# Kernel optimization log

Measured on AMD Instinct MI355X. Metric: run time of the kernel, lower is better.

## Reference

```python
import jax, jax.numpy as jnp
import numpy as np

N, IN, H, OUT, C = 1024, 64, 64, 64, 32
EPS = 1e-5   # SAKELayer.epsilon
INF = 1e5    # SAKELayer.inf


def _w(key, i, o, scale=1.0):
    return jax.random.normal(key, (i, o), jnp.float32) * (scale / np.sqrt(i))


def setup_inputs() -> dict:
    key = jax.random.key(0)
    ks = jax.random.split(key, 16)
    return dict(
        h=jax.random.normal(ks[0], (N, IN), jnp.float32),
        x=jax.random.normal(ks[1], (N, 3), jnp.float32),
        # edge model (ConcatenationFilter): Linear(2*IN+1,H), SiLU, Linear(H,H)
        ew1=_w(ks[2], 2 * IN + 1, H), eb1=jnp.zeros((H,), jnp.float32),
        ew2=_w(ks[3], H, H), eb2=jnp.zeros((H,), jnp.float32),
        # node_mlp: Linear(2H+IN,H), SiLU, Linear(H,OUT)
        nw1=_w(ks[4], 2 * H + IN, H), nb1=jnp.zeros((H,), jnp.float32),
        nw2=_w(ks[5], H, OUT), nb2=jnp.zeros((OUT,), jnp.float32),
        # coordinate_mlp: Linear(H,H), SiLU, Linear(H,1,bias=False) xavier gain 1e-3
        cw1=_w(ks[6], H, H), cb1=jnp.zeros((H,), jnp.float32),
        cw2=_w(ks[7], H, 1, scale=1e-3),
        # semantic_attention_mlp: Linear(H,1), LeakyReLU
        aw=_w(ks[8], H, 1), ab=jnp.zeros((1,), jnp.float32),
        # coefficients_mlp: Linear(H,H), SiLU, Linear(H,C)
        fw1=_w(ks[9], H, H), fb1=jnp.zeros((H,), jnp.float32),
        fw2=_w(ks[10], H, C), fb2=jnp.zeros((C,), jnp.float32),
        # post_norm_mlp: Linear(C,H), SiLU, Linear(H,H)
        pw1=_w(ks[11], C, H), pb1=jnp.zeros((H,), jnp.float32),
        pw2=_w(ks[12], H, H), pb2=jnp.zeros((H,), jnp.float32),
        log_gamma=jnp.array(0.0, jnp.float32),
    )


def reference(h, x, ew1, eb1, ew2, eb2, nw1, nb1, nw2, nb2, cw1, cb1, cw2,
              aw, ab, fw1, fb1, fw2, fb2, pw1, pb1, pw2, pb2, log_gamma):
    n, d_in = h.shape
    silu = jax.nn.silu
    eye = jnp.eye(n, dtype=h.dtype)[:, :, None]                    # [n,n,1]

    x_minus_xt = x[:, None, :] - x[None, :, :]                     # [n,n,3]
    norm = jnp.sqrt(jnp.sum(x_minus_xt ** 2, -1, keepdims=True) + EPS)  # [n,n,1]

    h_cat_ht = jnp.concatenate(
        [jnp.broadcast_to(h[:, None, :], (n, n, d_in)),
         jnp.broadcast_to(h[None, :, :], (n, n, d_in))], -1)       # [n,n,2*IN]

    # edge model: MLP over concat(features, distance)
    e_in = jnp.concatenate([h_cat_ht, norm], -1)                   # [n,n,2*IN+1]
    h_e = silu(e_in @ ew1 + eb1) @ ew2 + eb2                       # [n,n,H]

    # euclidean attention over neighbors j (diag masked by +INF distance)
    att_e = jax.nn.softmax(-(norm + INF * eye) * jnp.exp(log_gamma), axis=1)
    # semantic attention
    att_s = jax.nn.softmax(jax.nn.leaky_relu(h_e @ aw + ab) - INF * eye, axis=1)
    comb = att_e * att_s
    comb = comb / (jnp.sum(comb, axis=1, keepdims=True) + EPS)     # [n,n,1]
    h_e_att = h_e * comb                                           # [n,n,H]

    # spatial attention: equivariant coefficient combinations
    coeff = silu(h_e_att @ fw1 + fb1) @ fw2 + fb2                  # [n,n,C]
    dirs = x_minus_xt / (norm + 1.0)                               # [n,n,3]
    combos = jnp.einsum('ijc,ijd->icd', coeff, dirs) / n           # mean over j -> [n,C,3]
    h_comb = silu(jnp.sum(combos ** 2, -1) @ pw1 + pb1) @ pw2 + pb2  # [n,H]

    # node update
    h_agg = jnp.sum(h_e_att, axis=1)                               # [n,H]
    node_in = jnp.concatenate([h, h_agg, h_comb], -1)              # [n,2H+IN]
    h_out = h + (silu(node_in @ nw1 + nb1) @ nw2 + nb2)            # residual

    # equivariant coordinate update
    phi = silu(h_e @ cw1 + cb1) @ cw2                              # [n,n,1]
    x_out = x + jnp.mean(x_minus_xt * phi, axis=1)                 # [n,3]
    return h_out, x_out
```

## Files before the change

### kernel.cpp

```cpp
#include <hip/hip_runtime.h>
#include <hip/hip_bf16.h>

#define NN 1024
#define LSTR 72
#define EPSV 1e-5f
#define BIGINF 1e5f

typedef __attribute__((ext_vector_type(8))) short short8;
typedef __attribute__((ext_vector_type(4))) short short4v;
typedef __attribute__((ext_vector_type(4))) float f32x4;

__device__ __forceinline__ float siluf(float v) {
    return v * __builtin_amdgcn_rcpf(1.0f + __expf(-v));
}
__device__ __forceinline__ float pnorm(float dx, float dy, float dz) {
    return sqrtf(dx * dx + dy * dy + dz * dz + EPSV);
}
__device__ __forceinline__ float wsum(float v) {
#pragma unroll
    for (int off = 32; off > 0; off >>= 1) v += __shfl_xor(v, off, 64);
    return v;
}
__device__ __forceinline__ float red16(float v) {
    v += __shfl_xor(v, 1, 64); v += __shfl_xor(v, 2, 64);
    v += __shfl_xor(v, 4, 64); v += __shfl_xor(v, 8, 64);
    return v;
}
__device__ __forceinline__ float redquad(float v) {
    v += __shfl_xor(v, 16, 64); v += __shfl_xor(v, 32, 64);
    return v;
}
__device__ __forceinline__ short f2bs(float v) {
    __hip_bfloat16 b = __float2bfloat16(v);
    return *reinterpret_cast<short*>(&b);
}
__device__ __forceinline__ short f2bt(float v) {
    return (short)(__float_as_uint(v) >> 16);
}

__global__ void kA(const float* __restrict__ h, const float* __restrict__ ew1,
                   const float* __restrict__ eb1, const float* __restrict__ ew2,
                   const float* __restrict__ cw1, const float* __restrict__ fw1,
                   const float* __restrict__ fw2, const float* __restrict__ aw,
                   const float* __restrict__ ab, const float* __restrict__ eb2,
                   float* __restrict__ HA, float* __restrict__ HB,
                   float* __restrict__ HBT, short* __restrict__ ew2T,
                   short* __restrict__ cw1T, short* __restrict__ fw1T,
                   short* __restrict__ fw2T, float* __restrict__ wsv,
                   float* __restrict__ svb) {
    const int b = blockIdx.x;
    const int o = threadIdx.x;
    if (b < NN) {
        const int i = b;
        float hv = h[i * 64 + o];
        float a = 0.f, bb = eb1[o];
#pragma unroll
        for (int k = 0; k < 64; k++) {
            float hk = __shfl(hv, k, 64);
            a += hk * ew1[k * 64 + o];
            bb += hk * ew1[(64 + k) * 64 + o];
        }
        HA[i * 64 + o] = a;
        HB[i * 64 + o] = bb;
        HBT[o * NN + i] = bb;
    } else if (b < NN + 64) {
        const int r = b - NN;
        ew2T[r * 64 + o] = f2bs(ew2[o * 64 + r]);
        cw1T[r * 64 + o] = f2bs(cw1[o * 64 + r]);
        fw1T[r * 64 + o] = f2bs(fw1[o * 64 + r]);
        if (r < 32) fw2T[r * 64 + o] = f2bs(fw2[o * 32 + r]);
    } else {
        float s = 0.f;
#pragma unroll
        for (int q = 0; q < 64; q++) s += ew2[o * 64 + q] * aw[q];
        wsv[o] = s;
        float e = wsum(eb2[o] * aw[o]);
        if (o == 0) svb[0] = e + ab[0];
    }
}

__global__ __launch_bounds__(256) void kBn(
    const float* __restrict__ x, const float* __restrict__ ew1,
    const float* __restrict__ HA, const float* __restrict__ HBT,
    const float* __restrict__ wsv, const float* __restrict__ svb,
    const float* __restrict__ lg, float* __restrict__ ls,
    float* __restrict__ rowm, float* __restrict__ rowd) {
    const int i = blockIdx.x;
    const int t = threadIdx.x;
    const float* HAi = HA + i * 64;
    const float* w1 = ew1 + 128 * 64;
    const float gamma = __expf(lg[0]);
    const float svb0 = svb[0];
    const float xi0 = x[i * 3 + 0], xi1 = x[i * 3 + 1], xi2 = x[i * 3 + 2];

    float4 xa = ((const float4*)x)[3 * t + 0];
    float4 xb = ((const float4*)x)[3 * t + 1];
    float4 xc = ((const float4*)x)[3 * t + 2];
    float nrm[4], le[4], lv[4];
    {
        float dx0 = xi0 - xa.x, dy0 = xi1 - xa.y, dz0 = xi2 - xa.z;
        float dx1 = xi0 - xa.w, dy1 = xi1 - xb.x, dz1 = xi2 - xb.y;
        float dx2 = xi0 - xb.z, dy2 = xi1 - xb.w, dz2 = xi2 - xc.x;
        float dx3 = xi0 - xc.y, dy3 = xi1 - xc.z, dz3 = xi2 - xc.w;
        nrm[0] = pnorm(dx0, dy0, dz0);
        nrm[1] = pnorm(dx1, dy1, dz1);
        nrm[2] = pnorm(dx2, dy2, dz2);
        nrm[3] = pnorm(dx3, dy3, dz3);
    }
    float d0 = 0.f, d1 = 0.f, d2 = 0.f, d3 = 0.f;
#pragma unroll 8
    for (int k = 0; k < 64; k++) {
        float4 hb = *(const float4*)&HBT[k * NN + 4 * t];
        float hk = HAi[k], w1k = w1[k], wv = wsv[k];
        d0 += siluf(hk + hb.x + nrm[0] * w1k) * wv;
        d1 += siluf(hk + hb.y + nrm[1] * w1k) * wv;
        d2 += siluf(hk + hb.z + nrm[2] * w1k) * wv;
        d3 += siluf(hk + hb.w + nrm[3] * w1k) * wv;
    }
    float me = -3.0e38f, ms = -3.0e38f;
    float4 svo;
    {
        float dd[4] = {d0, d1, d2, d3};
#pragma unroll
        for (int m = 0; m < 4; m++) {
            int j = 4 * t + m;
            float sv = dd[m] + svb0;
            sv = sv >= 0.f ? sv : 0.01f * sv;
            if (j == i) sv -= BIGINF;
            lv[m] = sv;
            le[m] = -(nrm[m] + (j == i ? BIGINF : 0.f)) * gamma;
            me = fmaxf(me, le[m]);
            ms = fmaxf(ms, lv[m]);
        }
        svo.x = lv[0]; svo.y = lv[1]; svo.z = lv[2]; svo.w = lv[3];
    }
    *(float4*)&ls[(size_t)i * NN + 4 * t] = svo;

    __shared__ float sm[4], ss[4], s1[4], s2[4], s3[4];
#pragma unroll
    for (int off = 32; off > 0; off >>= 1) {
        me = fmaxf(me, __shfl_xor(me, off, 64));
        ms = fmaxf(ms, __shfl_xor(ms, off, 64));
    }
    const int w = t >> 6;
    if ((t & 63) == 0) { sm[w] = me; ss[w] = ms; }
    __syncthreads();
    me = fmaxf(fmaxf(sm[0], sm[1]), fmaxf(sm[2], sm[3]));
    ms = fmaxf(fmaxf(ss[0], ss[1]), fmaxf(ss[2], ss[3]));
    float Se = 0.f, Ss = 0.f, Sq = 0.f;
#pragma unroll
    for (int m = 0; m < 4; m++) {
        float ee = __expf(le[m] - me);
        float es = __expf(lv[m] - ms);
        Se += ee; Ss += es; Sq += ee * es;
    }
    Se = wsum(Se); Ss = wsum(Ss); Sq = wsum(Sq);
    if ((t & 63) == 0) { s1[w] = Se; s2[w] = Ss; s3[w] = Sq; }
    __syncthreads();
    if (t == 0) {
        rowm[i] = me + ms;
        rowd[i] = (s3[0] + s3[1] + s3[2] + s3[3]) +
                  EPSV * (s1[0] + s1[1] + s1[2] + s1[3]) * (s2[0] + s2[1] + s2[2] + s2[3]);
    }
}

__device__ __forceinline__ void stageW(const short* __restrict__ g, short* s,
                                       int tid, int rows) {
    for (int c = tid; c < rows * 16; c += 512) {
        int r = c >> 4, q = c & 15;
        *(short4v*)&s[r * LSTR + q * 4] = *(const short4v*)&g[r * 64 + q * 4];
    }
}

__global__ __launch_bounds__(512) void kD(
    const float* __restrict__ x, const float* __restrict__ ew1,
    const float* __restrict__ eb2, const float* __restrict__ cb1,
    const float* __restrict__ cw2, const float* __restrict__ fb1,
    const float* __restrict__ fb2, const float* __restrict__ lg,
    const float* __restrict__ HA, const float* __restrict__ HB,
    const short* __restrict__ ew2T, const short* __restrict__ cw1T,
    const short* __restrict__ fw1T, const short* __restrict__ fw2T,
    const float* __restrict__ ls, const float* __restrict__ rowm,
    const float* __restrict__ rowd, float* __restrict__ hagg,
    float* __restrict__ combos, float* __restrict__ xupd) {
    __shared__ __align__(16) short sWe[64 * LSTR];
    __shared__ __align__(16) short sWf[64 * LSTR];
    __shared__ __align__(16) short sW2[32 * LSTR];
    __shared__ __align__(16) short sScr[16][16 * LSTR];
    __shared__ float sHag[64], sCombos[96], sXupd[3];

    const int tid = threadIdx.x;
    const int i = blockIdx.x;
    const int lane = tid & 63, w = tid >> 6;
    const int col = lane & 15, quad = lane >> 4;

    stageW(ew2T, sWe, tid, 64);
    stageW(fw1T, sWf, tid, 64);
    stageW(fw2T, sW2, tid, 32);
    if (tid < 64) sHag[tid] = 0.f;
    else if (tid < 160) sCombos[tid - 64] = 0.f;
    else if (tid < 163) sXupd[tid - 160] = 0.f;

    short* scr0 = sScr[2 * w];
    short* scr1 = sScr[2 * w + 1];
    const float gamma = __expf(lg[0]);

    float w1r[2][8], har[2][8];
#pragma unroll
    for (int kb = 0; kb < 2; kb++)
#pragma unroll
        for (int t = 0; t < 8; t++) {
            w1r[kb][t] = ew1[128 * 64 + kb * 32 + quad * 8 + t];
            har[kb][t] = HA[i * 64 + kb * 32 + quad * 8 + t];
        }
    float eb[4], cbv[4], cwv[4], fbv[4];
#pragma unroll
    for (int nb = 0; nb < 4; nb++) {
        eb[nb] = eb2[nb * 16 + col];
        cbv[nb] = cb1[nb * 16 + col];
        cwv[nb] = cw2[nb * 16 + col];
        fbv[nb] = fb1[nb * 16 + col];
    }
    float fb2v[2] = {fb2[col], fb2[16 + col]};
    const float rm = rowm[i];
    const float invd = 1.0f / rowd[i];
    const float xi0 = x[i * 3 + 0], xi1 = x[i * 3 + 1], xi2 = x[i * 3 + 2];
    const float* lsi = ls + (size_t)i * NN;
    __syncthreads();

#pragma unroll 1
    for (int jt = 0; jt < 4; jt++) {
        const int r0 = jt * 256 + w * 16 + col;
        const int r1 = r0 + 128;
        float dx0 = xi0 - x[r0 * 3 + 0], dy0 = xi1 - x[r0 * 3 + 1], dz0 = xi2 - x[r0 * 3 + 2];
        float dx1 = xi0 - x[r1 * 3 + 0], dy1 = xi1 - x[r1 * 3 + 1], dz1 = xi2 - x[r1 * 3 + 2];
        float nr0 = pnorm(dx0, dy0, dz0), nr1 = pnorm(dx1, dy1, dz1);
        float iv0 = __builtin_amdgcn_rcpf(nr0 + 1.0f), iv1 = __builtin_amdgcn_rcpf(nr1 + 1.0f);
        float fx0 = dx0 * iv0, fy0 = dy0 * iv0, fz0 = dz0 * iv0;
        float fx1 = dx1 * iv1, fy1 = dy1 * iv1, fz1 = dz1 * iv1;
        float le0 = -(nr0 + (r0 == i ? BIGINF : 0.f)) * gamma;
        float le1 = -(nr1 + (r1 == i ? BIGINF : 0.f)) * gamma;
        float cb0 = __expf(le0 + lsi[r0] - rm) * invd;
        float cb1f = __expf(le1 + lsi[r1] - rm) * invd;

        short8 af0[2], af1[2];
#pragma unroll
        for (int kb = 0; kb < 2; kb++) {
            const float* hb0 = &HB[r0 * 64 + kb * 32 + quad * 8];
            const float* hb1 = &HB[r1 * 64 + kb * 32 + quad * 8];
#pragma unroll
            for (int t = 0; t < 8; t++) {
                af0[kb][t] = f2bt(siluf(har[kb][t] + hb0[t] + nr0 * w1r[kb][t]));
                af1[kb][t] = f2bt(siluf(har[kb][t] + hb1[t] + nr1 * w1r[kb][t]));
            }
        }
        f32x4 ac0[4] = {{0.f,0.f,0.f,0.f},{0.f,0.f,0.f,0.f},{0.f,0.f,0.f,0.f},{0.f,0.f,0.f,0.f}};
        f32x4 ac1[4] = {{0.f,0.f,0.f,0.f},{0.f,0.f,0.f,0.f},{0.f,0.f,0.f,0.f},{0.f,0.f,0.f,0.f}};
#pragma unroll
        for (int kb = 0; kb < 2; kb++) {
#pragma unroll
            for (int nb = 0; nb < 4; nb++) {
                short8 b = *(const short8*)&sWe[(nb * 16 + col) * LSTR + kb * 32 + quad * 8];
                ac0[nb] = __builtin_amdgcn_mfma_f32_16x16x32_bf16(af0[kb], b, ac0[nb], 0, 0, 0);
                ac1[nb] = __builtin_amdgcn_mfma_f32_16x16x32_bf16(af1[kb], b, ac1[nb], 0, 0, 0);
            }
        }
        {
            float cm0[4], cm1[4];
#pragma unroll
            for (int reg = 0; reg < 4; reg++) {
                cm0[reg] = __shfl(cb0, quad * 4 + reg, 64);
                cm1[reg] = __shfl(cb1f, quad * 4 + reg, 64);
            }
#pragma unroll
            for (int nb = 0; nb < 4; nb++) {
                float v = 0.f;
#pragma unroll
                for (int reg = 0; reg < 4; reg++) {
                    float h0 = ac0[nb][reg] + eb[nb];
                    float h1 = ac1[nb][reg] + eb[nb];
                    scr0[(quad * 4 + reg) * LSTR + nb * 16 + col] = f2bt(h0);
                    scr1[(quad * 4 + reg) * LSTR + nb * 16 + col] = f2bt(h1);
                    v += h0 * cm0[reg] + h1 * cm1[reg];
                }
                v = redquad(v);
                if (quad == 0) atomicAdd(&sHag[nb * 16 + col], v);
            }
        }
        short8 a00 = *(const short8*)&scr0[col * LSTR + quad * 8];
        short8 a01 = *(const short8*)&scr0[col * LSTR + 32 + quad * 8];
        short8 a10 = *(const short8*)&scr1[col * LSTR + quad * 8];
        short8 a11 = *(const short8*)&scr1[col * LSTR + 32 + quad * 8];

        {
            f32x4 p0[4] = {{0.f,0.f,0.f,0.f},{0.f,0.f,0.f,0.f},{0.f,0.f,0.f,0.f},{0.f,0.f,0.f,0.f}};
            f32x4 p1[4] = {{0.f,0.f,0.f,0.f},{0.f,0.f,0.f,0.f},{0.f,0.f,0.f,0.f},{0.f,0.f,0.f,0.f}};
#pragma unroll
            for (int nb = 0; nb < 4; nb++) {
                short8 b0 = *(const short8*)&cw1T[(nb * 16 + col) * 64 + quad * 8];
                short8 b1 = *(const short8*)&cw1T[(nb * 16 + col) * 64 + 32 + quad * 8];
                p0[nb] = __builtin_amdgcn_mfma_f32_16x16x32_bf16(a00, b0, p0[nb], 0, 0, 0);
                p0[nb] = __builtin_amdgcn_mfma_f32_16x16x32_bf16(a01, b1, p0[nb], 0, 0, 0);
                p1[nb] = __builtin_amdgcn_mfma_f32_16x16x32_bf16(a10, b0, p1[nb], 0, 0, 0);
                p1[nb] = __builtin_amdgcn_mfma_f32_16x16x32_bf16(a11, b1, p1[nb], 0, 0, 0);
            }
            float xa0 = 0.f, xa1 = 0.f, xa2 = 0.f;
#pragma unroll
            for (int reg = 0; reg < 4; reg++) {
                float ph0 = 0.f, ph1 = 0.f;
#pragma unroll
                for (int nb = 0; nb < 4; nb++) {
                    ph0 += siluf(p0[nb][reg] + cbv[nb]) * cwv[nb];
                    ph1 += siluf(p1[nb][reg] + cbv[nb]) * cwv[nb];
                }
                ph0 = red16(ph0); ph1 = red16(ph1);
                float t0x = __shfl(dx0, quad * 4 + reg, 64);
                float t0y = __shfl(dy0, quad * 4 + reg, 64);
                float t0z = __shfl(dz0, quad * 4 + reg, 64);
                float t1x = __shfl(dx1, quad * 4 + reg, 64);
                float t1y = __shfl(dy1, quad * 4 + reg, 64);
                float t1z = __shfl(dz1, quad * 4 + reg, 64);
                if (col == 0) {
                    xa0 += ph0 * t0x + ph1 * t1x;
                    xa1 += ph0 * t0y + ph1 * t1y;
                    xa2 += ph0 * t0z + ph1 * t1z;
                }
            }
            xa0 = wsum(xa0); xa1 = wsum(xa1); xa2 = wsum(xa2);
            if (lane == 0) {
                atomicAdd(&sXupd[0], xa0);
                atomicAdd(&sXupd[1], xa1);
                atomicAdd(&sXupd[2], xa2);
            }
        }

        {
            f32x4 v0[4] = {{0.f,0.f,0.f,0.f},{0.f,0.f,0.f,0.f},{0.f,0.f,0.f,0.f},{0.f,0.f,0.f,0.f}};
            f32x4 v1[4] = {{0.f,0.f,0.f,0.f},{0.f,0.f,0.f,0.f},{0.f,0.f,0.f,0.f},{0.f,0.f,0.f,0.f}};
#pragma unroll
            for (int nb = 0; nb < 4; nb++) {
                short8 b0 = *(const short8*)&sWf[(nb * 16 + col) * LSTR + quad * 8];
                short8 b1 = *(const short8*)&sWf[(nb * 16 + col) * LSTR + 32 + quad * 8];
                v0[nb] = __builtin_amdgcn_mfma_f32_16x16x32_bf16(a00, b0, v0[nb], 0, 0, 0);
                v0[nb] = __builtin_amdgcn_mfma_f32_16x16x32_bf16(a01, b1, v0[nb], 0, 0, 0);
                v1[nb] = __builtin_amdgcn_mfma_f32_16x16x32_bf16(a10, b0, v1[nb], 0, 0, 0);
                v1[nb] = __builtin_amdgcn_mfma_f32_16x16x32_bf16(a11, b1, v1[nb], 0, 0, 0);
            }
            float cm0[4], cm1[4];
#pragma unroll
            for (int reg = 0; reg < 4; reg++) {
                cm0[reg] = __shfl(cb0, quad * 4 + reg, 64);
                cm1[reg] = __shfl(cb1f, quad * 4 + reg, 64);
            }
#pragma unroll
            for (int reg = 0; reg < 4; reg++) {
#pragma unroll
                for (int nb = 0; nb < 4; nb++) {
                    scr0[(quad * 4 + reg) * LSTR + nb * 16 + col] =
                        f2bt(siluf(cm0[reg] * v0[nb][reg] + fbv[nb]));
                    scr1[(quad * 4 + reg) * LSTR + nb * 16 + col] =
                        f2bt(siluf(cm1[reg] * v1[nb][reg] + fbv[nb]));
                }
            }
        }
        short8 wa00 = *(const short8*)&scr0[col * LSTR + quad * 8];
        short8 wa01 = *(const short8*)&scr0[col * LSTR + 32 + quad * 8];
        short8 wa10 = *(const short8*)&scr1[col * LSTR + quad * 8];
        short8 wa11 = *(const short8*)&scr1[col * LSTR + 32 + quad * 8];

        {
            f32x4 c0[2] = {{0.f,0.f,0.f,0.f},{0.f,0.f,0.f,0.f}};
            f32x4 c1[2] = {{0.f,0.f,0.f,0.f},{0.f,0.f,0.f,0.f}};
#pragma unroll
            for (int nb = 0; nb < 2; nb++) {
                short8 b0 = *(const short8*)&sW2[(nb * 16 + col) * LSTR + quad * 8];
                short8 b1 = *(const short8*)&sW2[(nb * 16 + col) * LSTR + 32 + quad * 8];
                c0[nb] = __builtin_amdgcn_mfma_f32_16x16x32_bf16(wa00, b0, c0[nb], 0, 0, 0);
                c0[nb] = __builtin_amdgcn_mfma_f32_16x16x32_bf16(wa01, b1, c0[nb], 0, 0, 0);
                c1[nb] = __builtin_amdgcn_mfma_f32_16x16x32_bf16(wa10, b0, c1[nb], 0, 0, 0);
                c1[nb] = __builtin_amdgcn_mfma_f32_16x16x32_bf16(wa11, b1, c1[nb], 0, 0, 0);
            }
#pragma unroll
            for (int nb = 0; nb < 2; nb++) {
                float px = 0.f, py = 0.f, pz = 0.f;
#pragma unroll
                for (int reg = 0; reg < 4; reg++) {
                    float cf0 = c0[nb][reg] + fb2v[nb];
                    float cf1 = c1[nb][reg] + fb2v[nb];
                    float t0x = __shfl(fx0, quad * 4 + reg, 64);
                    float t0y = __shfl(fy0, quad * 4 + reg, 64);
                    float t0z = __shfl(fz0, quad * 4 + reg, 64);
                    float t1x = __shfl(fx1, quad * 4 + reg, 64);
                    float t1y = __shfl(fy1, quad * 4 + reg, 64);
                    float t1z = __shfl(fz1, quad * 4 + reg, 64);
                    px += cf0 * t0x + cf1 * t1x;
                    py += cf0 * t0y + cf1 * t1y;
                    pz += cf0 * t0z + cf1 * t1z;
                }
                px = redquad(px); py = redquad(py); pz = redquad(pz);
                if (quad == 0) {
                    int c = nb * 16 + col;
                    atomicAdd(&sCombos[c * 3 + 0], px);
                    atomicAdd(&sCombos[c * 3 + 1], py);
                    atomicAdd(&sCombos[c * 3 + 2], pz);
                }
            }
        }
    }
    __syncthreads();
    if (tid < 64) hagg[i * 64 + tid] = sHag[tid];
    else if (tid < 160) combos[i * 96 + tid - 64] = sCombos[tid - 64];
    else if (tid < 163) xupd[i * 3 + tid - 160] = sXupd[tid - 160];
}

__global__ void kE(const float* __restrict__ h, const float* __restrict__ x,
                   const float* __restrict__ nw1, const float* __restrict__ nb1,
                   const float* __restrict__ nw2, const float* __restrict__ nb2,
                   const float* __restrict__ pw1, const float* __restrict__ pb1,
                   const float* __restrict__ pw2, const float* __restrict__ pb2,
                   const float* __restrict__ hagg, const float* __restrict__ combos,
                   const float* __restrict__ xupd, float* __restrict__ out) {
    const int i = blockIdx.x, o = threadIdx.x;
    const float invN = 1.0f / (float)NN;
    float r = 0.f;
    if (o < 32) {
        float v0 = combos[i * 96 + o * 3 + 0] * invN;
        float v1 = combos[i * 96 + o * 3 + 1] * invN;
        float v2 = combos[i * 96 + o * 3 + 2] * invN;
        r = v0 * v0 + v1 * v1 + v2 * v2;
    }
    float t1 = pb1[o];
#pragma unroll
    for (int k = 0; k < 32; k++) t1 += __shfl(r, k, 64) * pw1[k * 64 + o];
    t1 = siluf(t1);
    float hc = pb2[o];
#pragma unroll
    for (int k = 0; k < 64; k++) hc += __shfl(t1, k, 64) * pw2[k * 64 + o];
    float hi = h[i * 64 + o];
    float ha = hagg[i * 64 + o];
    float t2 = nb1[o];
#pragma unroll
    for (int k = 0; k < 64; k++) t2 += __shfl(hi, k, 64) * nw1[k * 64 + o];
#pragma unroll
    for (int k = 0; k < 64; k++) t2 += __shfl(ha, k, 64) * nw1[(64 + k) * 64 + o];
#pragma unroll
    for (int k = 0; k < 64; k++) t2 += __shfl(hc, k, 64) * nw1[(128 + k) * 64 + o];
    t2 = siluf(t2);
    float ho = hi + nb2[o];
#pragma unroll
    for (int k = 0; k < 64; k++) ho += __shfl(t2, k, 64) * nw2[k * 64 + o];
    out[i * 64 + o] = ho;
    if (o < 3)
        out[NN * 64 + i * 3 + o] = x[i * 3 + o] + xupd[i * 3 + o] * invN;
}

extern "C" void kernel_launch(void* const* d_in, const int* in_sizes, int n_in,
                              void* d_out, int out_size, void* d_ws, size_t ws_size,
                              hipStream_t stream) {
    (void)in_sizes; (void)n_in; (void)out_size; (void)ws_size;
    const float* h   = (const float*)d_in[0];
    const float* x   = (const float*)d_in[1];
    const float* ew1 = (const float*)d_in[2];
    const float* eb1 = (const float*)d_in[3];
    const float* ew2 = (const float*)d_in[4];
    const float* eb2 = (const float*)d_in[5];
    const float* nw1 = (const float*)d_in[6];
    const float* nb1 = (const float*)d_in[7];
    const float* nw2 = (const float*)d_in[8];
    const float* nb2 = (const float*)d_in[9];
    const float* cw1 = (const float*)d_in[10];
    const float* cb1 = (const float*)d_in[11];
    const float* cw2 = (const float*)d_in[12];
    const float* aw  = (const float*)d_in[13];
    const float* ab  = (const float*)d_in[14];
    const float* fw1 = (const float*)d_in[15];
    const float* fb1 = (const float*)d_in[16];
    const float* fw2 = (const float*)d_in[17];
    const float* fb2 = (const float*)d_in[18];
    const float* pw1 = (const float*)d_in[19];
    const float* pb1 = (const float*)d_in[20];
    const float* pw2 = (const float*)d_in[21];
    const float* pb2 = (const float*)d_in[22];
    const float* lg  = (const float*)d_in[23];
    float* out = (float*)d_out;

    float* W      = (float*)d_ws;
    float* ls     = W;
    float* HA     = ls + (size_t)NN * NN;
    float* HB     = HA + NN * 64;
    float* HBT    = HB + NN * 64;
    float* rowm   = HBT + NN * 64;
    float* rowd   = rowm + NN;
    float* hagg   = rowd + NN;
    float* combos = hagg + NN * 64;
    float* xupd   = combos + NN * 96;
    float* wsv    = xupd + NN * 3;
    float* svb    = wsv + 64;
    short* ew2T   = (short*)(svb + 4);
    short* cw1T   = ew2T + 64 * 64;
    short* fw1T   = cw1T + 64 * 64;
    short* fw2T   = fw1T + 64 * 64;

    kA<<<NN + 65, 64, 0, stream>>>(h, ew1, eb1, ew2, cw1, fw1, fw2, aw, ab, eb2,
                                   HA, HB, HBT, ew2T, cw1T, fw1T, fw2T, wsv, svb);
    kBn<<<NN, 256, 0, stream>>>(x, ew1, HA, HBT, wsv, svb, lg, ls, rowm, rowd);
    kD<<<NN, 512, 0, stream>>>(x, ew1, eb2, cb1, cw2, fb1, fb2, lg, HA, HB,
                               ew2T, cw1T, fw1T, fw2T, ls, rowm, rowd,
                               hagg, combos, xupd);
    kE<<<NN, 64, 0, stream>>>(h, x, nw1, nb1, nw2, nb2, pw1, pb1, pw2, pb2,
                              hagg, combos, xupd, out);
}
```

Before: 282.5 us.

## Factor final linear layers out of per-edge loop via linearity of sums

The last coefficient layer (fw2) and the coordinate output projection (cw2) are linear, so the change accumulates per-node sums of activations times direction vectors inside the edge loop. It then applies fw2/fb2 and cw2 once per node in the final kernel. This removes the per-edge fw2 MFMA pass, its scratch round-trip, and per-tile cross-lane reductions and shared atomics, which are now done once at loop end. In exchange it keeps more accumulator registers live (occupancy hinted via launch bounds), adds more shuffles per tile, and moves a small matvec into the last kernel.

```diff
diff --git a/kernel.cpp b/kernel.cpp
--- a/kernel.cpp
+++ b/kernel.cpp
@@ -19,11 +19,6 @@
 __device__ __forceinline__ float wsum(float v) {
 #pragma unroll
     for (int off = 32; off > 0; off >>= 1) v += __shfl_xor(v, off, 64);
-    return v;
-}
-__device__ __forceinline__ float red16(float v) {
-    v += __shfl_xor(v, 1, 64); v += __shfl_xor(v, 2, 64);
-    v += __shfl_xor(v, 4, 64); v += __shfl_xor(v, 8, 64);
     return v;
 }
 __device__ __forceinline__ float redquad(float v) {
@@ -172,22 +167,20 @@
     }
 }
 
-__global__ __launch_bounds__(512) void kD(
+__global__ __launch_bounds__(512, 4) void kD(
     const float* __restrict__ x, const float* __restrict__ ew1,
     const float* __restrict__ eb2, const float* __restrict__ cb1,
-    const float* __restrict__ cw2, const float* __restrict__ fb1,
-    const float* __restrict__ fb2, const float* __restrict__ lg,
+    const float* __restrict__ fb1, const float* __restrict__ lg,
     const float* __restrict__ HA, const float* __restrict__ HB,
     const short* __restrict__ ew2T, const short* __restrict__ cw1T,
-    const short* __restrict__ fw1T, const short* __restrict__ fw2T,
+    const short* __restrict__ fw1T,
     const float* __restrict__ ls, const float* __restrict__ rowm,
     const float* __restrict__ rowd, float* __restrict__ hagg,
-    float* __restrict__ combos, float* __restrict__ xupd) {
+    float* __restrict__ Gw, float* __restrict__ H2w, float* __restrict__ sdw) {
     __shared__ __align__(16) short sWe[64 * LSTR];
     __shared__ __align__(16) short sWf[64 * LSTR];
-    __shared__ __align__(16) short sW2[32 * LSTR];
     __shared__ __align__(16) short sScr[16][16 * LSTR];
-    __shared__ float sHag[64], sCombos[96], sXupd[3];
+    __shared__ float sHag[64], sG[192], sH2[192], sSd[3];
 
     const int tid = threadIdx.x;
     const int i = blockIdx.x;
@@ -196,36 +189,31 @@
 
     stageW(ew2T, sWe, tid, 64);
     stageW(fw1T, sWf, tid, 64);
-    stageW(fw2T, sW2, tid, 32);
     if (tid < 64) sHag[tid] = 0.f;
-    else if (tid < 160) sCombos[tid - 64] = 0.f;
-    else if (tid < 163) sXupd[tid - 160] = 0.f;
+    else if (tid < 256) sG[tid - 64] = 0.f;
+    else if (tid < 448) sH2[tid - 256] = 0.f;
+    else if (tid < 451) sSd[tid - 448] = 0.f;
 
     short* scr0 = sScr[2 * w];
     short* scr1 = sScr[2 * w + 1];
     const float gamma = __expf(lg[0]);
 
-    float w1r[2][8], har[2][8];
-#pragma unroll
-    for (int kb = 0; kb < 2; kb++)
-#pragma unroll
-        for (int t = 0; t < 8; t++) {
-            w1r[kb][t] = ew1[128 * 64 + kb * 32 + quad * 8 + t];
-            har[kb][t] = HA[i * 64 + kb * 32 + quad * 8 + t];
-        }
-    float eb[4], cbv[4], cwv[4], fbv[4];
+    float eb[4], cbv[4], fbv[4];
 #pragma unroll
     for (int nb = 0; nb < 4; nb++) {
         eb[nb] = eb2[nb * 16 + col];
         cbv[nb] = cb1[nb * 16 + col];
-        cwv[nb] = cw2[nb * 16 + col];
         fbv[nb] = fb1[nb * 16 + col];
     }
-    float fb2v[2] = {fb2[col], fb2[16 + col]};
     const float rm = rowm[i];
     const float invd = 1.0f / rowd[i];
     const float xi0 = x[i * 3 + 0], xi1 = x[i * 3 + 1], xi2 = x[i * 3 + 2];
     const float* lsi = ls + (size_t)i * NN;
+
+    float hagA[4] = {0.f, 0.f, 0.f, 0.f};
+    float Ga[12]  = {0.f, 0.f, 0.f, 0.f, 0.f, 0.f, 0.f, 0.f, 0.f, 0.f, 0.f, 0.f};
+    float H2a[12] = {0.f, 0.f, 0.f, 0.f, 0.f, 0.f, 0.f, 0.f, 0.f, 0.f, 0.f, 0.f};
+    float sdx = 0.f, sdy = 0.f, sdz = 0.f;
     __syncthreads();
 
 #pragma unroll 1
@@ -236,8 +224,9 @@
         float dx1 = xi0 - x[r1 * 3 + 0], dy1 = xi1 - x[r1 * 3 + 1], dz1 = xi2 - x[r1 * 3 + 2];
         float nr0 = pnorm(dx0, dy0, dz0), nr1 = pnorm(dx1, dy1, dz1);
         float iv0 = __builtin_amdgcn_rcpf(nr0 + 1.0f), iv1 = __builtin_amdgcn_rcpf(nr1 + 1.0f);
-        float fx0 = dx0 * iv0, fy0 = dy0 * iv0, fz0 = dz0 * iv0;
-        float fx1 = dx1 * iv1, fy1 = dy1 * iv1, fz1 = dz1 * iv1;
+        sdx += dx0 * iv0 + dx1 * iv1;
+        sdy += dy0 * iv0 + dy1 * iv1;
+        sdz += dz0 * iv0 + dz1 * iv1;
         float le0 = -(nr0 + (r0 == i ? BIGINF : 0.f)) * gamma;
         float le1 = -(nr1 + (r1 == i ? BIGINF : 0.f)) * gamma;
         float cb0 = __expf(le0 + lsi[r0] - rm) * invd;
@@ -246,12 +235,15 @@
         short8 af0[2], af1[2];
 #pragma unroll
         for (int kb = 0; kb < 2; kb++) {
+            const float* hA  = &HA[i * 64 + kb * 32 + quad * 8];
+            const float* wr  = &ew1[128 * 64 + kb * 32 + quad * 8];
             const float* hb0 = &HB[r0 * 64 + kb * 32 + quad * 8];
             const float* hb1 = &HB[r1 * 64 + kb * 32 + quad * 8];
 #pragma unroll
             for (int t = 0; t < 8; t++) {
-                af0[kb][t] = f2bt(siluf(har[kb][t] + hb0[t] + nr0 * w1r[kb][t]));
-                af1[kb][t] = f2bt(siluf(har[kb][t] + hb1[t] + nr1 * w1r[kb][t]));
+                float ha = hA[t], wk = wr[t];
+                af0[kb][t] = f2bt(siluf(ha + hb0[t] + nr0 * wk));
+                af1[kb][t] = f2bt(siluf(ha + hb1[t] + nr1 * wk));
             }
         }
         f32x4 ac0[4] = {{0.f,0.f,0.f,0.f},{0.f,0.f,0.f,0.f},{0.f,0.f,0.f,0.f},{0.f,0.f,0.f,0.f}};
@@ -265,26 +257,21 @@
                 ac1[nb] = __builtin_amdgcn_mfma_f32_16x16x32_bf16(af1[kb], b, ac1[nb], 0, 0, 0);
             }
         }
-        {
-            float cm0[4], cm1[4];
+        float cm0[4], cm1[4];
+#pragma unroll
+        for (int reg = 0; reg < 4; reg++) {
+            cm0[reg] = __shfl(cb0, quad * 4 + reg, 64);
+            cm1[reg] = __shfl(cb1f, quad * 4 + reg, 64);
+        }
+#pragma unroll
+        for (int nb = 0; nb < 4; nb++) {
 #pragma unroll
             for (int reg = 0; reg < 4; reg++) {
-                cm0[reg] = __shfl(cb0, quad * 4 + reg, 64);
-                cm1[reg] = __shfl(cb1f, quad * 4 + reg, 64);
-            }
-#pragma unroll
-            for (int nb = 0; nb < 4; nb++) {
-                float v = 0.f;
-#pragma unroll
-                for (int reg = 0; reg < 4; reg++) {
-                    float h0 = ac0[nb][reg] + eb[nb];
-                    float h1 = ac1[nb][reg] + eb[nb];
-                    scr0[(quad * 4 + reg) * LSTR + nb * 16 + col] = f2bt(h0);
-                    scr1[(quad * 4 + reg) * LSTR + nb * 16 + col] = f2bt(h1);
-                    v += h0 * cm0[reg] + h1 * cm1[reg];
-                }
-                v = redquad(v);
-                if (quad == 0) atomicAdd(&sHag[nb * 16 + col], v);
+                float h0 = ac0[nb][reg] + eb[nb];
+                float h1 = ac1[nb][reg] + eb[nb];
+                scr0[(quad * 4 + reg) * LSTR + nb * 16 + col] = f2bt(h0);
+                scr1[(quad * 4 + reg) * LSTR + nb * 16 + col] = f2bt(h1);
+                hagA[nb] += h0 * cm0[reg] + h1 * cm1[reg];
             }
         }
         short8 a00 = *(const short8*)&scr0[col * LSTR + quad * 8];
@@ -304,33 +291,19 @@
                 p1[nb] = __builtin_amdgcn_mfma_f32_16x16x32_bf16(a10, b0, p1[nb], 0, 0, 0);
                 p1[nb] = __builtin_amdgcn_mfma_f32_16x16x32_bf16(a11, b1, p1[nb], 0, 0, 0);
             }
-            float xa0 = 0.f, xa1 = 0.f, xa2 = 0.f;
 #pragma unroll
             for (int reg = 0; reg < 4; reg++) {
-                float ph0 = 0.f, ph1 = 0.f;
+                int sl = quad * 4 + reg;
+                float t0x = __shfl(dx0, sl, 64), t0y = __shfl(dy0, sl, 64), t0z = __shfl(dz0, sl, 64);
+                float t1x = __shfl(dx1, sl, 64), t1y = __shfl(dy1, sl, 64), t1z = __shfl(dz1, sl, 64);
 #pragma unroll
                 for (int nb = 0; nb < 4; nb++) {
-                    ph0 += siluf(p0[nb][reg] + cbv[nb]) * cwv[nb];
-                    ph1 += siluf(p1[nb][reg] + cbv[nb]) * cwv[nb];
+                    float s0 = siluf(p0[nb][reg] + cbv[nb]);
+                    float s1 = siluf(p1[nb][reg] + cbv[nb]);
+                    H2a[nb * 3 + 0] += s0 * t0x + s1 * t1x;
+                    H2a[nb * 3 + 1] += s0 * t0y + s1 * t1y;
+                    H2a[nb * 3 + 2] += s0 * t0z + s1 * t1z;
                 }
-                ph0 = red16(ph0); ph1 = red16(ph1);
-                float t0x = __shfl(dx0, quad * 4 + reg, 64);
-                float t0y = __shfl(dy0, quad * 4 + reg, 64);
-                float t0z = __shfl(dz0, quad * 4 + reg, 64);
-                float t1x = __shfl(dx1, quad * 4 + reg, 64);
-                float t1y = __shfl(dy1, quad * 4 + reg, 64);
-                float t1z = __shfl(dz1, quad * 4 + reg, 64);
-                if (col == 0) {
-                    xa0 += ph0 * t0x + ph1 * t1x;
-                    xa1 += ph0 * t0y + ph1 * t1y;
-                    xa2 += ph0 * t0z + ph1 * t1z;
-                }
-            }
-            xa0 = wsum(xa0); xa1 = wsum(xa1); xa2 = wsum(xa2);
-            if (lane == 0) {
-                atomicAdd(&sXupd[0], xa0);
-                atomicAdd(&sXupd[1], xa1);
-                atomicAdd(&sXupd[2], xa2);
             }
         }
 
@@ -346,71 +319,54 @@
                 v1[nb] = __builtin_amdgcn_mfma_f32_16x16x32_bf16(a10, b0, v1[nb], 0, 0, 0);
                 v1[nb] = __builtin_amdgcn_mfma_f32_16x16x32_bf16(a11, b1, v1[nb], 0, 0, 0);
             }
-            float cm0[4], cm1[4];
 #pragma unroll
             for (int reg = 0; reg < 4; reg++) {
-                cm0[reg] = __shfl(cb0, quad * 4 + reg, 64);
-                cm1[reg] = __shfl(cb1f, quad * 4 + reg, 64);
-            }
-#pragma unroll
-            for (int reg = 0; reg < 4; reg++) {
+                int sl = quad * 4 + reg;
+                float ti0 = __shfl(iv0, sl, 64), ti1 = __shfl(iv1, sl, 64);
+                float f0x = __shfl(dx0, sl, 64) * ti0;
+                float f0y = __shfl(dy0, sl, 64) * ti0;
+                float f0z = __shfl(dz0, sl, 64) * ti0;
+                float f1x = __shfl(dx1, sl, 64) * ti1;
+                float f1y = __shfl(dy1, sl, 64) * ti1;
+                float f1z = __shfl(dz1, sl, 64) * ti1;
 #pragma unroll
                 for (int nb = 0; nb < 4; nb++) {
-                    scr0[(quad * 4 + reg) * LSTR + nb * 16 + col] =
-                        f2bt(siluf(cm0[reg] * v0[nb][reg] + fbv[nb]));
-                    scr1[(quad * 4 + reg) * LSTR + nb * 16 + col] =
-                        f2bt(siluf(cm1[reg] * v1[nb][reg] + fbv[nb]));
+                    float w0 = siluf(cm0[reg] * v0[nb][reg] + fbv[nb]);
+                    float w1 = siluf(cm1[reg] * v1[nb][reg] + fbv[nb]);
+                    Ga[nb * 3 + 0] += w0 * f0x + w1 * f1x;
+                    Ga[nb * 3 + 1] += w0 * f0y + w1 * f1y;
+                    Ga[nb * 3 + 2] += w0 * f0z + w1 * f1z;
                 }
             }
         }
-        short8 wa00 = *(const short8*)&scr0[col * LSTR + quad * 8];
-        short8 wa01 = *(const short8*)&scr0[col * LSTR + 32 + quad * 8];
-        short8 wa10 = *(const short8*)&scr1[col * LSTR + quad * 8];
-        short8 wa11 = *(const short8*)&scr1[col * LSTR + 32 + quad * 8];
-
-        {
-            f32x4 c0[2] = {{0.f,0.f,0.f,0.f},{0.f,0.f,0.f,0.f}};
-            f32x4 c1[2] = {{0.f,0.f,0.f,0.f},{0.f,0.f,0.f,0.f}};
-#pragma unroll
-            for (int nb = 0; nb < 2; nb++) {
-                short8 b0 = *(const short8*)&sW2[(nb * 16 + col) * LSTR + quad * 8];
-                short8 b1 = *(const short8*)&sW2[(nb * 16 + col) * LSTR + 32 + quad * 8];
-                c0[nb] = __builtin_amdgcn_mfma_f32_16x16x32_bf16(wa00, b0, c0[nb], 0, 0, 0);
-                c0[nb] = __builtin_amdgcn_mfma_f32_16x16x32_bf16(wa01, b1, c0[nb], 0, 0, 0);
-                c1[nb] = __builtin_amdgcn_mfma_f32_16x16x32_bf16(wa10, b0, c1[nb], 0, 0, 0);
-                c1[nb] = __builtin_amdgcn_mfma_f32_16x16x32_bf16(wa11, b1, c1[nb], 0, 0, 0);
-            }
-#pragma unroll
-            for (int nb = 0; nb < 2; nb++) {
-                float px = 0.f, py = 0.f, pz = 0.f;
-#pragma unroll
-                for (int reg = 0; reg < 4; reg++) {
-                    float cf0 = c0[nb][reg] + fb2v[nb];
-                    float cf1 = c1[nb][reg] + fb2v[nb];
-                    float t0x = __shfl(fx0, quad * 4 + reg, 64);
-                    float t0y = __shfl(fy0, quad * 4 + reg, 64);
-                    float t0z = __shfl(fz0, quad * 4 + reg, 64);
-                    float t1x = __shfl(fx1, quad * 4 + reg, 64);
-                    float t1y = __shfl(fy1, quad * 4 + reg, 64);
-                    float t1z = __shfl(fz1, quad * 4 + reg, 64);
-                    px += cf0 * t0x + cf1 * t1x;
-                    py += cf0 * t0y + cf1 * t1y;
-                    pz += cf0 * t0z + cf1 * t1z;
-                }
-                px = redquad(px); py = redquad(py); pz = redquad(pz);
-                if (quad == 0) {
-                    int c = nb * 16 + col;
-                    atomicAdd(&sCombos[c * 3 + 0], px);
-                    atomicAdd(&sCombos[c * 3 + 1], py);
-                    atomicAdd(&sCombos[c * 3 + 2], pz);
-                }
-            }
-        }
+    }
+
+#pragma unroll
+    for (int nb = 0; nb < 4; nb++) {
+        float v = redquad(hagA[nb]);
+        if (quad == 0) atomicAdd(&sHag[nb * 16 + col], v);
+    }
+#pragma unroll
+    for (int nb = 0; nb < 4; nb++) {
+#pragma unroll
+        for (int d = 0; d < 3; d++) {
+            float v = redquad(H2a[nb * 3 + d]);
+            if (quad == 0) atomicAdd(&sH2[(nb * 16 + col) * 3 + d], v);
+            float g = redquad(Ga[nb * 3 + d]);
+            if (quad == 0) atomicAdd(&sG[(nb * 16 + col) * 3 + d], g);
+        }
+    }
+    sdx = wsum(sdx); sdy = wsum(sdy); sdz = wsum(sdz);
+    if (lane == 0) {
+        atomicAdd(&sSd[0], 0.25f * sdx);
+        atomicAdd(&sSd[1], 0.25f * sdy);
+        atomicAdd(&sSd[2], 0.25f * sdz);
     }
     __syncthreads();
     if (tid < 64) hagg[i * 64 + tid] = sHag[tid];
-    else if (tid < 160) combos[i * 96 + tid - 64] = sCombos[tid - 64];
-    else if (tid < 163) xupd[i * 3 + tid - 160] = sXupd[tid - 160];
+    else if (tid < 256) Gw[i * 192 + tid - 64] = sG[tid - 64];
+    else if (tid < 448) H2w[i * 192 + tid - 256] = sH2[tid - 256];
+    else if (tid < 451) sdw[i * 3 + tid - 448] = sSd[tid - 448];
 }
 
 __global__ void kE(const float* __restrict__ h, const float* __restrict__ x,
@@ -418,16 +374,35 @@
                    const float* __restrict__ nw2, const float* __restrict__ nb2,
                    const float* __restrict__ pw1, const float* __restrict__ pb1,
                    const float* __restrict__ pw2, const float* __restrict__ pb2,
-                   const float* __restrict__ hagg, const float* __restrict__ combos,
-                   const float* __restrict__ xupd, float* __restrict__ out) {
+                   const float* __restrict__ fw2, const float* __restrict__ fb2,
+                   const float* __restrict__ cw2,
+                   const float* __restrict__ hagg, const float* __restrict__ Gw,
+                   const float* __restrict__ H2w, const float* __restrict__ sdw,
+                   float* __restrict__ out) {
     const int i = blockIdx.x, o = threadIdx.x;
     const float invN = 1.0f / (float)NN;
+    float cw2o = cw2[o];
+    float xd0 = wsum(cw2o * H2w[i * 192 + o * 3 + 0]);
+    float xd1 = wsum(cw2o * H2w[i * 192 + o * 3 + 1]);
+    float xd2 = wsum(cw2o * H2w[i * 192 + o * 3 + 2]);
+    float g0 = Gw[i * 192 + o * 3 + 0];
+    float g1 = Gw[i * 192 + o * 3 + 1];
+    float g2 = Gw[i * 192 + o * 3 + 2];
+    float v0 = 0.f, v1 = 0.f, v2 = 0.f;
+#pragma unroll
+    for (int m = 0; m < 64; m++) {
+        float fw = fw2[m * 32 + (o & 31)];
+        v0 += __shfl(g0, m, 64) * fw;
+        v1 += __shfl(g1, m, 64) * fw;
+        v2 += __shfl(g2, m, 64) * fw;
+    }
     float r = 0.f;
     if (o < 32) {
-        float v0 = combos[i * 96 + o * 3 + 0] * invN;
-        float v1 = combos[i * 96 + o * 3 + 1] * invN;
-        float v2 = combos[i * 96 + o * 3 + 2] * invN;
-        r = v0 * v0 + v1 * v1 + v2 * v2;
+        float fb = fb2[o];
+        float u0 = (v0 + fb * sdw[i * 3 + 0]) * invN;
+        float u1 = (v1 + fb * sdw[i * 3 + 1]) * invN;
+        float u2 = (v2 + fb * sdw[i * 3 + 2]) * invN;
+        r = u0 * u0 + u1 * u1 + u2 * u2;
     }
     float t1 = pb1[o];
 #pragma unroll
@@ -450,8 +425,10 @@
 #pragma unroll
     for (int k = 0; k < 64; k++) ho += __shfl(t2, k, 64) * nw2[k * 64 + o];
     out[i * 64 + o] = ho;
-    if (o < 3)
-        out[NN * 64 + i * 3 + o] = x[i * 3 + o] + xupd[i * 3 + o] * invN;
+    if (o < 3) {
+        float xdv = o == 0 ? xd0 : (o == 1 ? xd1 : xd2);
+        out[NN * 64 + i * 3 + o] = x[i * 3 + o] + xdv * invN;
+    }
 }
 
 extern "C" void kernel_launch(void* const* d_in, const int* in_sizes, int n_in,
@@ -500,13 +477,16 @@
     short* cw1T   = ew2T + 64 * 64;
     short* fw1T   = cw1T + 64 * 64;
     short* fw2T   = fw1T + 64 * 64;
+    float* Gw     = (float*)(fw2T + 32 * 64);
+    float* H2w    = Gw + (size_t)NN * 192;
+    float* sdw    = H2w + (size_t)NN * 192;
 
     kA<<<NN + 65, 64, 0, stream>>>(h, ew1, eb1, ew2, cw1, fw1, fw2, aw, ab, eb2,
                                    HA, HB, HBT, ew2T, cw1T, fw1T, fw2T, wsv, svb);
     kBn<<<NN, 256, 0, stream>>>(x, ew1, HA, HBT, wsv, svb, lg, ls, rowm, rowd);
-    kD<<<NN, 512, 0, stream>>>(x, ew1, eb2, cb1, cw2, fb1, fb2, lg, HA, HB,
-                               ew2T, cw1T, fw1T, fw2T, ls, rowm, rowd,
-                               hagg, combos, xupd);
+    kD<<<NN, 512, 0, stream>>>(x, ew1, eb2, cb1, fb1, lg, HA, HB,
+                               ew2T, cw1T, fw1T, ls, rowm, rowd,
+                               hagg, Gw, H2w, sdw);
     kE<<<NN, 64, 0, stream>>>(h, x, nw1, nb1, nw2, nb2, pw1, pb1, pw2, pb2,
-                              hagg, combos, xupd, out);
-}
+                              fw2, fb2, cw2, hagg, Gw, H2w, sdw, out);
+}
```

New measurement: 536.9 us. +90.1%, slower.
